# Kernel tuning notes

Measured on AMD Instinct MI355X. Metric: run time of the kernel, lower is better.

Reference implementation:

```python
import jax, jax.numpy as jnp
import numpy as np

IN_DIM = 1024
LOW_D_FF = 128
OUT_DIM = 1024
B = 8
S = 2048

def _xavier_normal(key, shape):
    fan_in, fan_out = shape[1], shape[0]
    std = float(np.sqrt(2.0 / (fan_in + fan_out)))
    return jax.random.normal(key, shape, dtype=jnp.float32) * std

def setup_inputs() -> dict:
    key = jax.random.key(0)
    kx, kk, kd, ku = jax.random.split(key, 4)
    x = jax.random.normal(kx, (B, S, IN_DIM), dtype=jnp.float32)
    k = jax.random.normal(kk, (B, LOW_D_FF), dtype=jnp.float32)
    D_matrix = _xavier_normal(kd, (IN_DIM * LOW_D_FF, LOW_D_FF))
    U_matrix = _xavier_normal(ku, (LOW_D_FF * OUT_DIM, LOW_D_FF))
    return {"x": x, "k": k, "D_matrix": D_matrix, "U_matrix": U_matrix}

def reference(x, k, D_matrix, U_matrix):
    # x: [B, S, in_dim], k: [B, low_d_ff]
    Bn = x.shape[0]
    low = k.shape[-1]
    # hypernetwork weight generation: per-sample D [B, in_dim, low], U [B, low, out_dim]
    D = jnp.einsum('pk,bk->bp', D_matrix, k).reshape(Bn, IN_DIM, low)
    U = jnp.einsum('pk,bk->bp', U_matrix, k).reshape(Bn, low, OUT_DIM)
    h = jax.nn.relu(jnp.einsum('bsd,bdl->bsl', x, D))
    return jnp.einsum('bsl,blo->bso', h, U)
```

## Files before the change

### kernel.cpp

```cpp
#include <hip/hip_runtime.h>
#include <hip/hip_bf16.h>
#include <stdint.h>

#define IN_DIM  1024
#define LOW     128
#define OUT_DIM 1024
#define BATCH   8
#define SEQ     2048

typedef unsigned short u16;
typedef short bf16x8 __attribute__((ext_vector_type(8)));
typedef unsigned short u16x4 __attribute__((ext_vector_type(4)));
typedef float f32x4 __attribute__((ext_vector_type(4)));

__device__ __forceinline__ u16 f2bf(float f) {
    union { float f; uint32_t u; } v;
    v.f = f;
    uint32_t u = v.u;
    return (u16)((u + 0x7fffu + ((u >> 16) & 1u)) >> 16);
}

__global__ __launch_bounds__(256, 1) void gen_half(const float* __restrict__ src,
                                                   const float* __restrict__ kv,
                                                   u16* __restrict__ outp,
                                                   int NTOT, int MTOT, int sh) {
    __shared__ u16 tb[8 * 8 * 32];

    int t = threadIdx.x;
    int rb = blockIdx.x;
    int m0 = (rb >> sh) * 32;
    int n0 = (rb & ((1 << sh) - 1)) * 8;

    int lane = t & 63, w = t >> 6;
    int lr = lane & 15;
    int hi = lane >> 4;

    bf16x8 bfrag[4];
#pragma unroll
    for (int ks = 0; ks < 4; ++ks)
#pragma unroll
        for (int j = 0; j < 8; ++j) {
            float kvf = (lr < 8) ? kv[lr * LOW + ks * 32 + hi * 8 + j] : 0.f;
            bfrag[ks][j] = (short)f2bf(kvf);
        }

    const float* abase = src +
        ((size_t)(m0 + w * 8 + (lr >> 3)) * NTOT + n0 + (lr & 7)) * 128 + hi * 8;
    size_t tstep = (size_t)2 * NTOT * 128;

    f32x4 L[4][8];
#pragma unroll
    for (int tau = 0; tau < 4; ++tau) {
        const float* rp = abase + (size_t)tau * tstep;
#pragma unroll
        for (int ks = 0; ks < 4; ++ks) {
            L[tau][2 * ks] =
                __builtin_nontemporal_load((const f32x4*)(rp + ks * 32));
            L[tau][2 * ks + 1] =
                __builtin_nontemporal_load((const f32x4*)(rp + ks * 32 + 4));
        }
    }

#pragma unroll
    for (int tau = 0; tau < 4; ++tau) {
        f32x4 acc = (f32x4){0.f, 0.f, 0.f, 0.f};
#pragma unroll
        for (int ks = 0; ks < 4; ++ks) {
            f32x4 v0 = L[tau][2 * ks], v1 = L[tau][2 * ks + 1];
            bf16x8 afr;
            afr[0] = (short)f2bf(v0.x); afr[1] = (short)f2bf(v0.y);
            afr[2] = (short)f2bf(v0.z); afr[3] = (short)f2bf(v0.w);
            afr[4] = (short)f2bf(v1.x); afr[5] = (short)f2bf(v1.y);
            afr[6] = (short)f2bf(v1.z); afr[7] = (short)f2bf(v1.w);
            acc = __builtin_amdgcn_mfma_f32_16x16x32_bf16(afr, bfrag[ks],
                                                          acc, 0, 0, 0);
        }
        if (lr < 8) {
#pragma unroll
            for (int j = 0; j < 4; ++j) {
                int r = hi * 4 + j;
                int mm = w * 8 + tau * 2 + (r >> 3);
                tb[lr * 256 + (r & 7) * 32 + mm] = f2bf(acc[j]);
            }
        }
    }

    __syncthreads();

    int c64 = t >> 2, q4 = t & 3;
    int bw = c64 >> 3, np = c64 & 7;
    bf16x8 v = *(const bf16x8*)(tb + bw * 256 + np * 32 + q4 * 8);
    *(bf16x8*)(outp + ((size_t)(bw * NTOT + n0 + np)) * MTOT + m0 + q4 * 8) = v;
}

__global__ __launch_bounds__(256) void fc1(const float* __restrict__ x,
                                           const u16* __restrict__ DgT,
                                           u16* __restrict__ h) {
    __shared__ u16 As[32][72];
    __shared__ u16 Bs[128][72];
    int t = threadIdx.x;
    int bid = blockIdx.x;
    int b = bid >> 6, st = bid & 63;
    int s0 = st * 32;
    const float* xb = x + ((size_t)b * SEQ + s0) * IN_DIM;
    const u16* Db = DgT + (size_t)b * LOW * IN_DIM;

    int w = t >> 6, lane = t & 63;
    int wm = w >> 1, wn = w & 1;
    int lr = lane & 15, hi = lane >> 4;

    f32x4 acc[4];
#pragma unroll
    for (int nf = 0; nf < 4; ++nf) acc[nf] = (f32x4){0.f, 0.f, 0.f, 0.f};

    int ar = t >> 3, ac = t & 7;
    int brt = t >> 3, bc = t & 7;

    for (int kt = 0; kt < IN_DIM / 64; ++kt) {
        int k0 = kt * 64;
#pragma unroll
        for (int i = 0; i < 2; ++i) {
            float4 v = *(const float4*)(xb + (size_t)ar * IN_DIM + k0 + ac * 4 + i * 32);
            u16x4 o;
            o.x = f2bf(v.x); o.y = f2bf(v.y); o.z = f2bf(v.z); o.w = f2bf(v.w);
            *(u16x4*)(&As[ar][ac * 4 + i * 32]) = o;
        }
#pragma unroll
        for (int i = 0; i < 4; ++i) {
            int row = brt + 32 * i;
            bf16x8 v = *(const bf16x8*)(Db + (size_t)row * IN_DIM + k0 + bc * 8);
            *(bf16x8*)(&Bs[row][bc * 8]) = v;
        }
        __syncthreads();
#pragma unroll
        for (int ks = 0; ks < 2; ++ks) {
            int kk = ks * 32 + hi * 8;
            bf16x8 af = *(const bf16x8*)(&As[wm * 16 + lr][kk]);
#pragma unroll
            for (int nf = 0; nf < 4; ++nf) {
                bf16x8 bf = *(const bf16x8*)(&Bs[wn * 64 + nf * 16 + lr][kk]);
                acc[nf] = __builtin_amdgcn_mfma_f32_16x16x32_bf16(af, bf, acc[nf], 0, 0, 0);
            }
        }
        __syncthreads();
    }
    u16* hb = h + ((size_t)b * SEQ + s0) * LOW;
#pragma unroll
    for (int nf = 0; nf < 4; ++nf) {
        int col = wn * 64 + nf * 16 + lr;
#pragma unroll
        for (int j = 0; j < 4; ++j) {
            int rrow = wm * 16 + hi * 4 + j;
            hb[(size_t)rrow * LOW + col] = f2bf(fmaxf(acc[nf][j], 0.f));
        }
    }
}

__global__ __launch_bounds__(256) void fc2(const u16* __restrict__ h,
                                           const u16* __restrict__ UgT,
                                           float* __restrict__ out) {
    __shared__ u16 As[128 * 128];
    __shared__ u16 Bs[128 * 128];
    int t = threadIdx.x;
    int bid = blockIdx.x;
    int b = bid >> 7, st = (bid >> 3) & 15, ot = bid & 7;
    int s0 = st * 128, o0 = ot * 128;
    const u16* hb = h + ((size_t)b * SEQ + s0) * LOW;
    const u16* Ub = UgT + ((size_t)b * OUT_DIM + o0) * LOW;

#pragma unroll
    for (int i = 0; i < 8; ++i) {
        int ch = i * 256 + t;
        int row = ch >> 4, c = ch & 15;
        int swc = c ^ (row & 7);
        *(bf16x8*)(As + row * 128 + swc * 8) = *(const bf16x8*)(hb + (size_t)ch * 8);
        *(bf16x8*)(Bs + row * 128 + swc * 8) = *(const bf16x8*)(Ub + (size_t)ch * 8);
    }
    __syncthreads();

    int w = t >> 6, lane = t & 63;
    int wm = w >> 1, wn = w & 1;
    int lr = lane & 15, lkc = (lane >> 4);

    f32x4 acc[4][4];
#pragma unroll
    for (int mf = 0; mf < 4; ++mf)
#pragma unroll
        for (int nf = 0; nf < 4; ++nf)
            acc[mf][nf] = (f32x4){0.f, 0.f, 0.f, 0.f};

#pragma unroll
    for (int ks = 0; ks < 4; ++ks) {
        bf16x8 af[4], bfr[4];
#pragma unroll
        for (int mf = 0; mf < 4; ++mf) {
            int row = wm * 64 + mf * 16 + lr;
            int swc = (ks * 4 + lkc) ^ (row & 7);
            af[mf] = *(const bf16x8*)(As + row * 128 + swc * 8);
        }
#pragma unroll
        for (int nf = 0; nf < 4; ++nf) {
            int row = wn * 64 + nf * 16 + lr;
            int swc = (ks * 4 + lkc) ^ (row & 7);
            bfr[nf] = *(const bf16x8*)(Bs + row * 128 + swc * 8);
        }
#pragma unroll
        for (int mf = 0; mf < 4; ++mf)
#pragma unroll
            for (int nf = 0; nf < 4; ++nf)
                acc[mf][nf] = __builtin_amdgcn_mfma_f32_16x16x32_bf16(
                    af[mf], bfr[nf], acc[mf][nf], 0, 0, 0);
    }

    float* ob = out + ((size_t)b * SEQ + s0) * OUT_DIM + o0;
#pragma unroll
    for (int mf = 0; mf < 4; ++mf)
#pragma unroll
        for (int nf = 0; nf < 4; ++nf) {
            int col = wn * 64 + nf * 16 + lr;
#pragma unroll
            for (int j = 0; j < 4; ++j) {
                int rrow = wm * 64 + mf * 16 + (lane >> 4) * 4 + j;
                ob[(size_t)rrow * OUT_DIM + col] = acc[mf][nf][j];
            }
        }
}

extern "C" void kernel_launch(void* const* d_in, const int* in_sizes, int n_in,
                              void* d_out, int out_size, void* d_ws, size_t ws_size,
                              hipStream_t stream) {
    const float* x  = (const float*)d_in[0];
    const float* kv = (const float*)d_in[1];
    const float* Dm = (const float*)d_in[2];
    const float* Um = (const float*)d_in[3];
    float* out = (float*)d_out;

    u16* DgT  = (u16*)d_ws;
    u16* UgT  = DgT + (size_t)BATCH * LOW * IN_DIM;
    u16* hbuf = UgT + (size_t)BATCH * OUT_DIM * LOW;

    gen_half<<<dim3(512), dim3(256), 0, stream>>>(Dm, kv, DgT, 128, 1024, 4);
    gen_half<<<dim3(512), dim3(256), 0, stream>>>(Um, kv, UgT, 1024, 128, 7);
    fc1<<<dim3(512), dim3(256), 0, stream>>>(x, DgT, hbuf);
    fc2<<<dim3(1024), dim3(256), 0, stream>>>(hbuf, UgT, out);
}
```

Baseline: 71.54 us.

## Stream hypernetwork weight tiles via global_load_lds double buffering in gen_half

Replaces gen_half's direct register loads of the large D/U matrices with asynchronous global-to-LDS loads (global_load_lds) into a per-wave double buffer. It uses an XOR swizzle and explicit waitcnt so the loads for the next tau overlap the conversion and MFMA of the current one. This is meant to ease register pressure from holding all 32 f32x4 loads at once and to keep the memory stream going in this bandwidth-bound weight-generation stage. It adds 64KB of LDS per block and drops the occupancy hint of 1, and the hand-coded waitcnt values must match the load counts exactly.

Result: slower. 74.44 us (+4.1%).

```diff
diff --git a/kernel.cpp b/kernel.cpp
--- a/kernel.cpp
+++ b/kernel.cpp
@@ -20,10 +20,15 @@
     return (u16)((u + 0x7fffu + ((u >> 16) & 1u)) >> 16);
 }
 
-__global__ __launch_bounds__(256, 1) void gen_half(const float* __restrict__ src,
-                                                   const float* __restrict__ kv,
-                                                   u16* __restrict__ outp,
-                                                   int NTOT, int MTOT, int sh) {
+#define WAIT_VM8   0x0F78
+#define WAIT_VM0   0x0F70
+#define WAIT_LGKM0 0xC07F
+
+__global__ __launch_bounds__(256) void gen_half(const float* __restrict__ src,
+                                                const float* __restrict__ kv,
+                                                u16* __restrict__ outp,
+                                                int NTOT, int MTOT, int sh) {
+    __shared__ float sbuf[4 * 2 * 2048];
     __shared__ u16 tb[8 * 8 * 32];
 
     int t = threadIdx.x;
@@ -34,6 +39,7 @@
     int lane = t & 63, w = t >> 6;
     int lr = lane & 15;
     int hi = lane >> 4;
+    int rsw = lr & 7;
 
     bf16x8 bfrag[4];
 #pragma unroll
@@ -44,29 +50,51 @@
             bfrag[ks][j] = (short)f2bf(kvf);
         }
 
-    const float* abase = src +
-        ((size_t)(m0 + w * 8 + (lr >> 3)) * NTOT + n0 + (lr & 7)) * 128 + hi * 8;
-    size_t tstep = (size_t)2 * NTOT * 128;
-
-    f32x4 L[4][8];
+    float* wbase = sbuf + w * 2 * 2048;
+
+#define STAGE(tau) {                                                          \
+    float* lb = wbase + ((tau) & 1) * 2048;                                   \
+    _Pragma("unroll")                                                         \
+    for (int i = 0; i < 8; ++i) {                                             \
+        int rt = i * 2 + (lane >> 5);                                         \
+        int ck = (lane & 31) ^ (rt & 7);                                      \
+        const float* ga = src +                                               \
+            ((size_t)(m0 + w * 8 + (tau) * 2 + (rt >> 3)) * NTOT              \
+             + n0 + (rt & 7)) * 128 + ck * 4;                                 \
+        __builtin_amdgcn_global_load_lds(                                     \
+            (const __attribute__((address_space(1))) void*)ga,                \
+            (__attribute__((address_space(3))) void*)(lb + i * 256), 16, 0, 0); \
+    }                                                                         \
+    __builtin_amdgcn_sched_barrier(0);                                        \
+}
+
+    STAGE(0)
+    STAGE(1)
+
 #pragma unroll
     for (int tau = 0; tau < 4; ++tau) {
-        const float* rp = abase + (size_t)tau * tstep;
+        if (tau < 3) __builtin_amdgcn_s_waitcnt(WAIT_VM8);
+        else         __builtin_amdgcn_s_waitcnt(WAIT_VM0);
+        __builtin_amdgcn_sched_barrier(0);
+
+        const float* tp = wbase + (tau & 1) * 2048 + lr * 128;
+        f32x4 va[4], vb[4];
 #pragma unroll
         for (int ks = 0; ks < 4; ++ks) {
-            L[tau][2 * ks] =
-                __builtin_nontemporal_load((const f32x4*)(rp + ks * 32));
-            L[tau][2 * ks + 1] =
-                __builtin_nontemporal_load((const f32x4*)(rp + ks * 32 + 4));
-        }
-    }
-
-#pragma unroll
-    for (int tau = 0; tau < 4; ++tau) {
+            int c0 = ks * 8 + hi * 2;
+            va[ks] = *(const f32x4*)(tp + ((c0 ^ rsw) * 4));
+            vb[ks] = *(const f32x4*)(tp + (((c0 + 1) ^ rsw) * 4));
+        }
+        __builtin_amdgcn_sched_barrier(0);
+        __builtin_amdgcn_s_waitcnt(WAIT_LGKM0);
+        __builtin_amdgcn_sched_barrier(0);
+
+        if (tau < 2) STAGE(tau + 2)
+
         f32x4 acc = (f32x4){0.f, 0.f, 0.f, 0.f};
 #pragma unroll
         for (int ks = 0; ks < 4; ++ks) {
-            f32x4 v0 = L[tau][2 * ks], v1 = L[tau][2 * ks + 1];
+            f32x4 v0 = va[ks], v1 = vb[ks];
             bf16x8 afr;
             afr[0] = (short)f2bf(v0.x); afr[1] = (short)f2bf(v0.y);
             afr[2] = (short)f2bf(v0.z); afr[3] = (short)f2bf(v0.w);
@@ -84,6 +112,7 @@
             }
         }
     }
+#undef STAGE
 
     __syncthreads();
 
```
